# Performance work log

Hardware: AMD Instinct MI355X
Metric: run time of the kernel (lower is better)

Reference implementation:

```python
import jax, jax.numpy as jnp
import numpy as np

H = 1024   # hidden size
NH = 16    # num heads
HD = H // NH  # 64


def setup_inputs() -> dict:
    key = jax.random.key(0)
    ks = jax.random.split(key, 8)
    B, S = 4, 2048
    scale = 0.02
    return {
        "hidden_states": jax.random.normal(ks[0], (B, S, H), jnp.float32),
        "attention_mask": jnp.zeros((B, 1, 1, S), jnp.float32),
        "Wq": jax.random.normal(ks[1], (H, H), jnp.float32) * scale,
        "bq": jnp.zeros((H,), jnp.float32),
        "Wk": jax.random.normal(ks[2], (H, H), jnp.float32) * scale,
        "bk": jnp.zeros((H,), jnp.float32),
        "Wv": jax.random.normal(ks[3], (H, H), jnp.float32) * scale,
        "bv": jnp.zeros((H,), jnp.float32),
    }


def reference(hidden_states, attention_mask, Wq, bq, Wk, bk, Wv, bv):
    B, S, _ = hidden_states.shape

    def split_heads(x):  # [B,S,H] -> [B,NH,S,HD]
        return x.reshape(B, S, NH, HD).transpose(0, 2, 1, 3)

    q = split_heads(hidden_states @ Wq.T + bq)
    k = split_heads(hidden_states @ Wk.T + bk)
    v = split_heads(hidden_states @ Wv.T + bv)

    # scores: [B,NH,S,S]
    scores = jnp.einsum("bhqd,bhkd->bhqk", q, k) / jnp.sqrt(jnp.float32(HD))
    scores = scores + attention_mask  # additive mask, broadcast [B,1,1,S]
    probs = jax.nn.softmax(scores, axis=-1)
    # dropout p=0.1 treated as identity (eval mode) for determinism
    ctx = jnp.einsum("bhqk,bhkd->bhqd", probs, v)  # [B,NH,S,HD]
    ctx = ctx.transpose(0, 2, 1, 3).reshape(B, S, H)  # [B,S,H]
    return ctx
```

## Files before the change

### kernel.cpp

```cpp
#include <hip/hip_runtime.h>
#include <hip/hip_bf16.h>
#include <math.h>


typedef __attribute__((ext_vector_type(8))) short short8;
typedef __attribute__((ext_vector_type(8))) __bf16 bf16x8;
typedef __attribute__((ext_vector_type(2))) __bf16 bf16x2;
typedef __attribute__((ext_vector_type(2))) float f32x2;
typedef __attribute__((ext_vector_type(4))) float f32x4;
typedef __attribute__((ext_vector_type(16))) float f32x16;
typedef __attribute__((ext_vector_type(2))) unsigned uint2v;

__device__ inline short f2bf(float f) {
    return __builtin_bit_cast(unsigned short, (__bf16)f);
}

__device__ inline unsigned packbf2(float lo, float hi) {
    bf16x2 v = {(__bf16)lo, (__bf16)hi};
    return __builtin_bit_cast(unsigned, v);
}

__device__ inline short8 pack8(f32x4 a, f32x4 b) {
    short8 r;
    r[0] = f2bf(a[0]); r[1] = f2bf(a[1]); r[2] = f2bf(a[2]); r[3] = f2bf(a[3]);
    r[4] = f2bf(b[0]); r[5] = f2bf(b[1]); r[6] = f2bf(b[2]); r[7] = f2bf(b[3]);
    return r;
}

__device__ inline void gl_lds16(const void* g, void* l) {
    __builtin_amdgcn_global_load_lds(
        (const __attribute__((address_space(1))) void*)g,
        (__attribute__((address_space(3))) void*)l, 16, 0, 0);
}

__device__ inline void plswap(unsigned& a, unsigned& b) {
    uint2v r = __builtin_amdgcn_permlane32_swap(a, b, false, false);
    a = r[0]; b = r[1];
}

__device__ inline float xhalf_add(float x) {
    unsigned a = __builtin_bit_cast(unsigned, x), b = a;
    plswap(a, b);
    return __builtin_bit_cast(float, a) + __builtin_bit_cast(float, b);
}

union PaFrag { unsigned u[4]; bf16x8 v; };

#define QSCALE 0.18033688f

__global__ void to_bf16(const float* __restrict__ hs,
                        const float* __restrict__ wq, const float* __restrict__ wk,
                        const float* __restrict__ wv,
                        short* __restrict__ hs_bf, short* __restrict__ w_bf) {
    int i = (blockIdx.x * 256 + threadIdx.x) * 8;
    if (i < 8388608) {
        f32x4 a = *(const f32x4*)(hs + i), b = *(const f32x4*)(hs + i + 4);
        *(short8*)(hs_bf + i) = pack8(a, b);
    } else {
        int j = i - 8388608;
        const float* w = (j < 1048576) ? wq : (j < 2097152 ? wk : wv);
        int o = j & 1048575;
        f32x4 a = *(const f32x4*)(w + o), b = *(const f32x4*)(w + o + 4);
        *(short8*)(w_bf + j) = pack8(a, b);
    }
}

__launch_bounds__(256, 2)
__global__ void qkv_gemm_bf(const short* __restrict__ hs_bf,
                            const short* __restrict__ w_bf,
                            const float* __restrict__ bq, const float* __restrict__ bk,
                            const float* __restrict__ bv,
                            short* __restrict__ q_ws, short* __restrict__ k_ws,
                            short* __restrict__ v_ws) {
    __shared__ short ldsAB[2][128 * 64];
    short* ldsA = ldsAB[0];
    short* ldsB = ldsAB[1];

    const int t = threadIdx.x;
    const int lane = t & 63;
    const int wid = t >> 6;
    const int nt = blockIdx.x;
    const int mt = blockIdx.y;
    const int mat = nt >> 3;
    const int o0 = (nt & 7) * 128;
    const int m0 = mt * 128;

    const short* W    = w_bf + mat * 1048576;
    const float* bias = (mat == 0) ? bq : (mat == 1) ? bk : bv;

    const int wm = wid >> 1, wn = wid & 1;

    f32x4 acc[4][4] = {};

    for (int kt = 0; kt < 16; ++kt) {
#pragma unroll
        for (int c = 0; c < 4; ++c) {
            int idx = c * 256 + t;
            int row = idx >> 3;
            int ch  = idx & 7;
            int kcol = kt * 64 + ((ch ^ (row & 7)) << 3);
            gl_lds16(hs_bf + (m0 + row) * 1024 + kcol, (char*)ldsA + idx * 16);
            gl_lds16(W     + (o0 + row) * 1024 + kcol, (char*)ldsB + idx * 16);
        }
        __syncthreads();

#pragma unroll
        for (int kk = 0; kk < 2; ++kk) {
            bf16x8 a[4], bfr[4];
            const int kbyte = (kk * 32 + ((lane >> 4) << 3)) * 2;
#pragma unroll
            for (int i = 0; i < 4; ++i) {
                int row = wm * 64 + i * 16 + (lane & 15);
                a[i] = *(const bf16x8*)((const char*)ldsA + row * 128 +
                                        (kbyte ^ ((row & 7) << 4)));
            }
#pragma unroll
            for (int j = 0; j < 4; ++j) {
                int row = wn * 64 + j * 16 + (lane & 15);
                bfr[j] = *(const bf16x8*)((const char*)ldsB + row * 128 +
                                          (kbyte ^ ((row & 7) << 4)));
            }
#pragma unroll
            for (int i = 0; i < 4; ++i)
#pragma unroll
                for (int j = 0; j < 4; ++j)
                    acc[i][j] = __builtin_amdgcn_mfma_f32_16x16x32_bf16(
                        a[i], bfr[j], acc[i][j], 0, 0, 0);
        }
        __syncthreads();
    }

    if (mat != 2) {
        const float sc = (mat == 0) ? QSCALE : 1.0f;
#pragma unroll
        for (int j = 0; j < 4; ++j) {
            int o = o0 + wn * 64 + j * 16 + (lane & 15);
            float bv_f = bias[o];
            int hh = o >> 6, d = o & 63;
            short* dst = (mat == 0) ? q_ws : k_ws;
#pragma unroll
            for (int i = 0; i < 4; ++i)
#pragma unroll
                for (int r = 0; r < 4; ++r) {
                    int m = m0 + wm * 64 + i * 16 + ((lane >> 4) << 2) + r;
                    int bb = m >> 11, s = m & 2047;
                    dst[((bb * 16 + hh) * 2048 + s) * 64 + d] =
                        f2bf((acc[i][j][r] + bv_f) * sc);
                }
        }
    } else {
        __syncthreads();
        short* ldsT = ldsAB[0];
#pragma unroll
        for (int j = 0; j < 4; ++j) {
            int o_l = wn * 64 + j * 16 + (lane & 15);
            float bv_f = bias[o0 + o_l];
#pragma unroll
            for (int i = 0; i < 4; ++i)
#pragma unroll
                for (int r = 0; r < 4; ++r) {
                    int m_l = wm * 64 + i * 16 + ((lane >> 4) << 2) + r;
                    ldsT[o_l * 128 +
                         ((((m_l >> 3) ^ (o_l & 15)) << 3) | (m_l & 7))] =
                        f2bf(acc[i][j][r] + bv_f);
                }
        }
        __syncthreads();
        const int bb = m0 >> 11, sbase = m0 & 2047;
#pragma unroll
        for (int c = 0; c < 8; ++c) {
            int id = c * 256 + t;
            int orow = id >> 4, mseg = id & 15;
            short8 v = *(const short8*)&ldsT[orow * 128 +
                                             ((mseg ^ (orow & 15)) << 3)];
            int o = o0 + orow;
            *(short8*)&v_ws[((bb * 16 + (o >> 6)) * 64 + (o & 63)) * 2048 +
                            sbase + mseg * 8] = v;
        }
    }
}

__launch_bounds__(256, 2)
__global__ void qkv_gemm_f32(const float* __restrict__ hs,
                             const float* __restrict__ Wq, const float* __restrict__ Wk,
                             const float* __restrict__ Wv,
                             const float* __restrict__ bq, const float* __restrict__ bk,
                             const float* __restrict__ bv,
                             short* __restrict__ q_ws, short* __restrict__ k_ws,
                             short* __restrict__ v_ws) {
    __shared__ short ldsA[128 * 64];
    __shared__ short ldsB[128 * 64];

    const int t = threadIdx.x;
    const int lane = t & 63;
    const int wid = t >> 6;
    const int nt = blockIdx.x;
    const int mt = blockIdx.y;
    const int mat = nt >> 3;
    const int o0 = (nt & 7) * 128;
    const int m0 = mt * 128;

    const float* W    = (mat == 0) ? Wq : (mat == 1) ? Wk : Wv;
    const float* bias = (mat == 0) ? bq : (mat == 1) ? bk : bv;

    const int wm = wid >> 1, wn = wid & 1;

    f32x4 acc[4][4] = {};

    for (int kt = 0; kt < 16; ++kt) {
#pragma unroll
        for (int c = 0; c < 4; ++c) {
            int idx = c * 256 + t;
            int row = idx >> 3;
            int ch  = idx & 7;
            const float* gA = hs + (m0 + row) * 1024 + kt * 64 + ch * 8;
            const float* gB = W  + (o0 + row) * 1024 + kt * 64 + ch * 8;
            f32x4 a0 = ((const f32x4*)gA)[0], a1 = ((const f32x4*)gA)[1];
            f32x4 b0 = ((const f32x4*)gB)[0], b1 = ((const f32x4*)gB)[1];
            int sw = (ch ^ (row & 7)) << 4;
            *(short8*)((char*)ldsA + row * 128 + sw) = pack8(a0, a1);
            *(short8*)((char*)ldsB + row * 128 + sw) = pack8(b0, b1);
        }
        __syncthreads();

#pragma unroll
        for (int kk = 0; kk < 2; ++kk) {
            bf16x8 a[4], bfr[4];
            const int kbyte = (kk * 32 + ((lane >> 4) << 3)) * 2;
#pragma unroll
            for (int i = 0; i < 4; ++i) {
                int row = wm * 64 + i * 16 + (lane & 15);
                a[i] = *(const bf16x8*)((const char*)ldsA + row * 128 +
                                        (kbyte ^ ((row & 7) << 4)));
            }
#pragma unroll
            for (int j = 0; j < 4; ++j) {
                int row = wn * 64 + j * 16 + (lane & 15);
                bfr[j] = *(const bf16x8*)((const char*)ldsB + row * 128 +
                                          (kbyte ^ ((row & 7) << 4)));
            }
#pragma unroll
            for (int i = 0; i < 4; ++i)
#pragma unroll
                for (int j = 0; j < 4; ++j)
                    acc[i][j] = __builtin_amdgcn_mfma_f32_16x16x32_bf16(
                        a[i], bfr[j], acc[i][j], 0, 0, 0);
        }
        __syncthreads();
    }

#pragma unroll
    for (int j = 0; j < 4; ++j) {
        int o = o0 + wn * 64 + j * 16 + (lane & 15);
        float bv_f = bias[o];
        int hh = o >> 6, d = o & 63;
#pragma unroll
        for (int i = 0; i < 4; ++i)
#pragma unroll
            for (int r = 0; r < 4; ++r) {
                int m = m0 + wm * 64 + i * 16 + ((lane >> 4) << 2) + r;
                int bb = m >> 11, s = m & 2047;
                if (mat == 0)
                    q_ws[((bb * 16 + hh) * 2048 + s) * 64 + d] =
                        f2bf((acc[i][j][r] + bv_f) * QSCALE);
                else if (mat == 1)
                    k_ws[((bb * 16 + hh) * 2048 + s) * 64 + d] =
                        f2bf(acc[i][j][r] + bv_f);
                else
                    v_ws[((bb * 16 + hh) * 64 + d) * 2048 + s] =
                        f2bf(acc[i][j][r] + bv_f);
            }
    }
}

__launch_bounds__(256, 4)
__global__ void attn(const short* __restrict__ q_ws, const short* __restrict__ k_ws,
                     const short* __restrict__ v_ws, const float* __restrict__ mask,
                     float* __restrict__ out) {
    __shared__ short ldsK[2][64 * 64];
    __shared__ short ldsV[2][64 * 64];
    __shared__ float ldsM[2048];

    const int t = threadIdx.x;
    const int lane = t & 63;
    const int wid = t >> 6;

    const int i = blockIdx.x;
    const int xl = i & 7;
    const int s_ = i >> 3;
    const int qt = s_ & 15;
    const int bh = ((s_ >> 4) << 3) + xl;
    const int b = bh >> 4, hh = bh & 15;
    const int qw = qt * 128 + wid * 32;

    const int q32 = lane & 31;
    const int h = lane >> 5;

    const int kr0 = t >> 3, kq0 = t & 7;
    const int kr1 = 32 + kr0;
    const short* ksrc0 = k_ws + (bh * 2048 + kr0) * 64 + ((kq0 ^ (kr0 & 7)) << 3);
    const short* ksrc1 = k_ws + (bh * 2048 + kr1) * 64 + ((kq0 ^ (kr1 & 7)) << 3);

    const int vr0 = t >> 3;
    const int vc0 = ((t & 7) ^ (vr0 & 7)) << 3;
    const int vr1 = 32 + vr0;
    const int vc1 = ((t & 7) ^ (vr1 & 7)) << 3;
    const short* vsrc0 = v_ws + (bh * 64 + vr0) * 2048 + vc0;
    const short* vsrc1 = v_ws + (bh * 64 + vr1) * 2048 + vc1;

#define STAGE(buf, T_)                                                           \
    do {                                                                         \
        gl_lds16(ksrc0 + (T_) * 4096, (char*)ldsK[buf] + t * 16);                \
        gl_lds16(ksrc1 + (T_) * 4096, (char*)ldsK[buf] + (256 + t) * 16);        \
        gl_lds16(vsrc0 + (T_) * 64,   (char*)ldsV[buf] + t * 16);                \
        gl_lds16(vsrc1 + (T_) * 64,   (char*)ldsV[buf] + (256 + t) * 16);        \
    } while (0)

    bf16x8 qf[4];
#pragma unroll
    for (int kc = 0; kc < 4; ++kc)
        qf[kc] = *(const bf16x8*)(q_ws + (bh * 2048 + qw + q32) * 64 +
                                  kc * 16 + 8 * h);

    STAGE(0, 0);
    {
        const float* mrow = mask + b * 2048;
        f32x4 a = *(const f32x4*)(mrow + t * 8);
        f32x4 c = *(const f32x4*)(mrow + t * 8 + 4);
#pragma unroll
        for (int j2 = 0; j2 < 4; ++j2) { a[j2] *= 1.44269504f; c[j2] *= 1.44269504f; }
        *(f32x4*)&ldsM[t * 8]     = a;
        *(f32x4*)&ldsM[t * 8 + 4] = c;
    }
    __syncthreads();

    f32x16 acc0 = {}, acc1 = {};
    float l_run = 0.f;

    for (int T = 0; T < 32; ++T) {
        const int cur = T & 1;
        STAGE(cur ^ 1, (T + 1) & 31);
        asm volatile("s_waitcnt vmcnt(4)" ::: "memory");
        __builtin_amdgcn_s_barrier();
        __builtin_amdgcn_sched_barrier(0);

        bf16x8 kf0[4], kf1[4];
        {
            const int row0 = q32, row1 = 32 + q32;
            const int sz0 = (row0 & 7) << 4, sz1 = (row1 & 7) << 4;
            const char* kb0 = (const char*)ldsK[cur] + row0 * 128;
            const char* kb1 = (const char*)ldsK[cur] + row1 * 128;
#pragma unroll
            for (int kc = 0; kc < 4; ++kc) {
                kf0[kc] = *(const bf16x8*)(kb0 + ((kc * 32 + 16 * h) ^ sz0));
                kf1[kc] = *(const bf16x8*)(kb1 + ((kc * 32 + 16 * h) ^ sz1));
            }
        }

        f32x16 s0 = {}, s1 = {};
        __builtin_amdgcn_s_setprio(1);
#pragma unroll
        for (int kc = 0; kc < 4; ++kc) {
            s0 = __builtin_amdgcn_mfma_f32_32x32x16_bf16(kf0[kc], qf[kc], s0, 0, 0, 0);
            s1 = __builtin_amdgcn_mfma_f32_32x32x16_bf16(kf1[kc], qf[kc], s1, 0, 0, 0);
        }
        __builtin_amdgcn_s_setprio(0);

        const float* mb0 = &ldsM[T * 64 + 4 * h];
        const float* mb1 = mb0 + 32;
#pragma unroll
        for (int j = 0; j < 8; ++j) {
            f32x2 mk0 = *(const f32x2*)(mb0 + 8 * (j >> 1) + 2 * (j & 1));
            f32x2 mk1 = *(const f32x2*)(mb1 + 8 * (j >> 1) + 2 * (j & 1));
            f32x2 t0 = (f32x2){s0[2 * j], s0[2 * j + 1]} + mk0;
            f32x2 t1 = (f32x2){s1[2 * j], s1[2 * j + 1]} + mk1;
            s0[2 * j]     = __builtin_amdgcn_exp2f(t0[0]);
            s0[2 * j + 1] = __builtin_amdgcn_exp2f(t0[1]);
            s1[2 * j]     = __builtin_amdgcn_exp2f(t1[0]);
            s1[2 * j + 1] = __builtin_amdgcn_exp2f(t1[1]);
        }

        {
            f32x2 c0 = (f32x2){s0[0], s0[1]}   + (f32x2){s0[2], s0[3]};
            f32x2 c1 = (f32x2){s0[4], s0[5]}   + (f32x2){s0[6], s0[7]};
            f32x2 c2 = (f32x2){s0[8], s0[9]}   + (f32x2){s0[10], s0[11]};
            f32x2 c3 = (f32x2){s0[12], s0[13]} + (f32x2){s0[14], s0[15]};
            f32x2 d0 = (f32x2){s1[0], s1[1]}   + (f32x2){s1[2], s1[3]};
            f32x2 d1 = (f32x2){s1[4], s1[5]}   + (f32x2){s1[6], s1[7]};
            f32x2 d2 = (f32x2){s1[8], s1[9]}   + (f32x2){s1[10], s1[11]};
            f32x2 d3 = (f32x2){s1[12], s1[13]} + (f32x2){s1[14], s1[15]};
            c0 += c1; c2 += c3; d0 += d1; d2 += d3;
            c0 += c2; d0 += d2;
            c0 += d0;
            l_run += xhalf_add(c0[0] + c0[1]);
        }

        PaFrag f0, f1, f2, f3;
        {
            unsigned a, bw;
            a = packbf2(s0[0], s0[1]);   bw = packbf2(s0[4], s0[5]);
            plswap(a, bw); f0.u[0] = a; f0.u[2] = bw;
            a = packbf2(s0[2], s0[3]);   bw = packbf2(s0[6], s0[7]);
            plswap(a, bw); f0.u[1] = a; f0.u[3] = bw;
            a = packbf2(s0[8], s0[9]);   bw = packbf2(s0[12], s0[13]);
            plswap(a, bw); f1.u[0] = a; f1.u[2] = bw;
            a = packbf2(s0[10], s0[11]); bw = packbf2(s0[14], s0[15]);
            plswap(a, bw); f1.u[1] = a; f1.u[3] = bw;
            a = packbf2(s1[0], s1[1]);   bw = packbf2(s1[4], s1[5]);
            plswap(a, bw); f2.u[0] = a; f2.u[2] = bw;
            a = packbf2(s1[2], s1[3]);   bw = packbf2(s1[6], s1[7]);
            plswap(a, bw); f2.u[1] = a; f2.u[3] = bw;
            a = packbf2(s1[8], s1[9]);   bw = packbf2(s1[12], s1[13]);
            plswap(a, bw); f3.u[0] = a; f3.u[2] = bw;
            a = packbf2(s1[10], s1[11]); bw = packbf2(s1[14], s1[15]);
            plswap(a, bw); f3.u[1] = a; f3.u[3] = bw;
        }

#define PVQ(ACC, N2)                                                             \
        do {                                                                     \
            int rowd = (N2) * 32 + q32;                                          \
            int swz = (rowd & 7) << 4;                                           \
            const char* vb = (const char*)ldsV[cur] + rowd * 128;                \
            bf16x8 v00 = *(const bf16x8*)(vb + ((16 * h) ^ swz));                \
            bf16x8 v01 = *(const bf16x8*)(vb + ((16 * h + 32) ^ swz));           \
            bf16x8 v10 = *(const bf16x8*)(vb + ((64 + 16 * h) ^ swz));           \
            bf16x8 v11 = *(const bf16x8*)(vb + ((64 + 16 * h + 32) ^ swz));      \
            ACC = __builtin_amdgcn_mfma_f32_32x32x16_bf16(f0.v, v00, ACC, 0, 0, 0); \
            ACC = __builtin_amdgcn_mfma_f32_32x32x16_bf16(f1.v, v01, ACC, 0, 0, 0); \
            ACC = __builtin_amdgcn_mfma_f32_32x32x16_bf16(f2.v, v10, ACC, 0, 0, 0); \
            ACC = __builtin_amdgcn_mfma_f32_32x32x16_bf16(f3.v, v11, ACC, 0, 0, 0); \
        } while (0)
        __builtin_amdgcn_s_setprio(1);
        PVQ(acc0, 0);
        PVQ(acc1, 1);
        __builtin_amdgcn_s_setprio(0);
#undef PVQ

        __builtin_amdgcn_s_barrier();
    }
#undef STAGE

    float linv = 1.f / l_run;
#pragma unroll
    for (int r = 0; r < 16; ++r) {
        int qs = (r & 3) + 8 * (r >> 2) + 4 * h;
        float rl = __shfl(linv, qs);
        float* orow = out + (b * 2048 + qw + qs) * 1024 + hh * 64;
        orow[q32]      = acc0[r] * rl;
        orow[32 + q32] = acc1[r] * rl;
    }
}

extern "C" void kernel_launch(void* const* d_in, const int* in_sizes, int n_in,
                              void* d_out, int out_size, void* d_ws, size_t ws_size,
                              hipStream_t stream) {
    const float* hs   = (const float*)d_in[0];
    const float* mask = (const float*)d_in[1];
    const float* Wq   = (const float*)d_in[2];
    const float* bq   = (const float*)d_in[3];
    const float* Wk   = (const float*)d_in[4];
    const float* bk   = (const float*)d_in[5];
    const float* Wv   = (const float*)d_in[6];
    const float* bv   = (const float*)d_in[7];
    float* out = (float*)d_out;

    short* q_ws = (short*)d_ws;
    short* k_ws = q_ws + 8388608;
    short* v_ws = k_ws + 8388608;

    dim3 blk(256);
    const size_t need = (size_t)(48 + 16 + 6) * 1024 * 1024;

    if (ws_size >= need) {
        short* hs_bf = v_ws + 8388608;
        short* w_bf  = hs_bf + 8388608;
        to_bf16<<<5632, blk, 0, stream>>>(hs, Wq, Wk, Wv, hs_bf, w_bf);
        dim3 g1(24, 64);
        qkv_gemm_bf<<<g1, blk, 0, stream>>>(hs_bf, w_bf, bq, bk, bv,
                                            q_ws, k_ws, v_ws);
    } else {
        dim3 g1(24, 64);
        qkv_gemm_f32<<<g1, blk, 0, stream>>>(hs, Wq, Wk, Wv, bq, bk, bv,
                                             q_ws, k_ws, v_ws);
    }

    dim3 g2(1024);
    attn<<<g2, blk, 0, stream>>>(q_ws, k_ws, v_ws, mask, out);
}
```

Measured before the change: 161.2 us.

## Double-buffer QKV GEMM LDS loads and remap block order for L2 locality

The QKV projection GEMM now double-buffers its LDS tiles. It issues the global-to-LDS loads for the next k-tile before computing on the current one, and waits with a partial vmcnt so load latency overlaps the MFMA work. Block indices are also remapped so that groups of blocks sharing rows or columns run close together, which should improve L2 reuse. This doubles LDS use to 64KB per block, which may reduce occupancy below the two blocks per CU that launch_bounds requests. On the last iteration it also issues a redundant reload of tile 15.

Result: no change. 161.2 us (-0.0%).

```diff
diff --git a/kernel.cpp b/kernel.cpp
--- a/kernel.cpp
+++ b/kernel.cpp
@@ -72,15 +72,17 @@
                             const float* __restrict__ bv,
                             short* __restrict__ q_ws, short* __restrict__ k_ws,
                             short* __restrict__ v_ws) {
-    __shared__ short ldsAB[2][128 * 64];
-    short* ldsA = ldsAB[0];
-    short* ldsB = ldsAB[1];
+    __shared__ short ldsS[2][2][128 * 64];
 
     const int t = threadIdx.x;
     const int lane = t & 63;
     const int wid = t >> 6;
-    const int nt = blockIdx.x;
-    const int mt = blockIdx.y;
+
+    const int L  = blockIdx.y * 24 + blockIdx.x;
+    const int L2 = (L & 7) * 192 + (L >> 3);
+    const int nt = L2 % 24;
+    const int mt = L2 / 24;
+
     const int mat = nt >> 3;
     const int o0 = (nt & 7) * 128;
     const int m0 = mt * 128;
@@ -92,17 +94,33 @@
 
     f32x4 acc[4][4] = {};
 
+#define GSTAGE(buf, kt_)                                                        \
+    do {                                                                        \
+        _Pragma("unroll")                                                       \
+        for (int c = 0; c < 4; ++c) {                                           \
+            int idx = c * 256 + t;                                              \
+            int row = idx >> 3;                                                 \
+            int ch  = idx & 7;                                                  \
+            int kcol = (kt_) * 64 + ((ch ^ (row & 7)) << 3);                    \
+            gl_lds16(hs_bf + (m0 + row) * 1024 + kcol,                          \
+                     (char*)ldsS[buf][0] + idx * 16);                           \
+            gl_lds16(W + (o0 + row) * 1024 + kcol,                              \
+                     (char*)ldsS[buf][1] + idx * 16);                           \
+        }                                                                       \
+    } while (0)
+
+    GSTAGE(0, 0);
+
     for (int kt = 0; kt < 16; ++kt) {
-#pragma unroll
-        for (int c = 0; c < 4; ++c) {
-            int idx = c * 256 + t;
-            int row = idx >> 3;
-            int ch  = idx & 7;
-            int kcol = kt * 64 + ((ch ^ (row & 7)) << 3);
-            gl_lds16(hs_bf + (m0 + row) * 1024 + kcol, (char*)ldsA + idx * 16);
-            gl_lds16(W     + (o0 + row) * 1024 + kcol, (char*)ldsB + idx * 16);
-        }
-        __syncthreads();
+        const int cur = kt & 1;
+        const int nxt = (kt < 15) ? (kt + 1) : 15;
+        GSTAGE(cur ^ 1, nxt);
+        asm volatile("s_waitcnt vmcnt(8)" ::: "memory");
+        __builtin_amdgcn_s_barrier();
+        __builtin_amdgcn_sched_barrier(0);
+
+        const short* ldsA = ldsS[cur][0];
+        const short* ldsB = ldsS[cur][1];
 
 #pragma unroll
         for (int kk = 0; kk < 2; ++kk) {
@@ -127,8 +145,9 @@
                     acc[i][j] = __builtin_amdgcn_mfma_f32_16x16x32_bf16(
                         a[i], bfr[j], acc[i][j], 0, 0, 0);
         }
-        __syncthreads();
-    }
+        __builtin_amdgcn_s_barrier();
+    }
+#undef GSTAGE
 
     if (mat != 2) {
         const float sc = (mat == 0) ? QSCALE : 1.0f;
@@ -150,7 +169,7 @@
         }
     } else {
         __syncthreads();
-        short* ldsT = ldsAB[0];
+        short* ldsT = (short*)ldsS;
 #pragma unroll
         for (int j = 0; j < 4; ++j) {
             int o_l = wn * 64 + j * 16 + (lane & 15);
```
